# Kernel tuning notes

Hardware: AMD Instinct MI355X
Metric: run time of the kernel (lower is better)

The kernel has to match this reference:

```python
import jax, jax.numpy as jnp
import numpy as np
from jax.ops import segment_sum

N_NODES = 100000


def _add_self_loops(edge_index, n):
    loop = jnp.arange(n, dtype=edge_index.dtype)
    src = jnp.concatenate([edge_index[0], loop])
    dst = jnp.concatenate([edge_index[1], loop])
    return src, dst


def gcn_conv(x, W, b, src, dst, n):
    # PyG GCNConv: h = x @ W, symmetric-normalized sum aggregation, + bias
    h = x @ W                                        # [N, out]
    deg = segment_sum(jnp.ones_like(dst, dtype=h.dtype), dst, num_segments=n)
    dinv = jnp.where(deg > 0, jax.lax.rsqrt(deg), 0.0)  # deg^-1/2, inf->0
    w = dinv[src] * dinv[dst]                        # [E]
    msg = h[src] * w[:, None]                        # gather + scale
    agg = segment_sum(msg, dst, num_segments=n)      # scatter-add
    return agg + b


def setup_inputs() -> dict:
    key = jax.random.key(0)
    ks = jax.random.split(key, 10)
    in_c, hid = 128, 64
    x = jax.random.normal(ks[0], (N_NODES, in_c), dtype=jnp.float32)
    edge_index = jax.random.randint(ks[1], (2, 3200000), 0, N_NODES, dtype=jnp.int64)
    s = 0.1
    return {
        "x": x,
        "edge_index": edge_index,
        "W1": jax.random.normal(ks[2], (in_c, hid), dtype=jnp.float32) * s,
        "b1": jnp.zeros((hid,), dtype=jnp.float32),
        "W2": jax.random.normal(ks[3], (hid, hid // 2), dtype=jnp.float32) * s,
        "b2": jnp.zeros((hid // 2,), dtype=jnp.float32),
        "fc_w": jax.random.normal(ks[4], (hid // 2, hid // 2), dtype=jnp.float32) * s,
        "fc_b": jnp.zeros((hid // 2,), dtype=jnp.float32),
        "out_w": jax.random.normal(ks[5], (hid // 2, 2), dtype=jnp.float32) * s,
        "out_b": jnp.zeros((2,), dtype=jnp.float32),
    }


def reference(x, edge_index, W1, b1, W2, b2, fc_w, fc_b, out_w, out_b):
    n = x.shape[0]
    src, dst = _add_self_loops(edge_index, n)
    h = jax.nn.relu(gcn_conv(x, W1, b1, src, dst, n))   # dropout: eval mode, identity
    h = jax.nn.relu(gcn_conv(h, W2, b2, src, dst, n))
    h = jax.nn.relu(h @ fc_w + fc_b)
    return h @ out_w + out_b                             # [N, 2] logits
```

## Files before the change

### kernel.cpp

```cpp
#include <hip/hip_runtime.h>

#define WG 256
#define BN 128
#define NBMAX 800
#define CHUNK 8192

typedef unsigned int uint32;

__device__ inline ushort f2bf(float f) {
  uint32 u = __float_as_uint(f);
  return (ushort)((u + 0x7fffu + ((u >> 16) & 1u)) >> 16);
}
__device__ inline float bflo(uint32 v) { return __uint_as_float(v << 16); }
__device__ inline float bfhi(uint32 v) { return __uint_as_float(v & 0xffff0000u); }

__device__ inline bool detect_i64(const uint32* ei) {
  uint32 acc = 0;
#pragma unroll
  for (int i = 0; i < 8; i++) acc |= ei[2 * i + 1];
  return acc == 0u;
}

__global__ __launch_bounds__(WG) void k_bin(const int* __restrict__ ei,
                                            int* __restrict__ cursor,
                                            uint32* __restrict__ pairs,
                                            int NB, int E, int CAP) {
  __shared__ int hc[NBMAX];
  __shared__ int curs[NBMAX];
  const int c = blockIdx.x;
  for (int b = threadIdx.x; b < NB; b += WG) hc[b] = 0;
  __syncthreads();
  const bool i64 = detect_i64((const uint32*)ei);
  const int e0 = c * CHUNK;
  for (int i = 0; i < CHUNK; i += WG) {
    int e = e0 + i + threadIdx.x;
    if (e < E) {
      int d = i64 ? ei[2 * (E + e)] : ei[E + e];
      atomicAdd(&hc[d / BN], 1);
    }
  }
  __syncthreads();
  for (int b = threadIdx.x; b < NB; b += WG) {
    int cnt = hc[b];
    int base = 0;
    if (cnt > 0) base = atomicAdd(&cursor[b], cnt);
    curs[b] = b * CAP + base;
  }
  __syncthreads();
  for (int i = 0; i < CHUNK; i += WG) {
    int e = e0 + i + threadIdx.x;
    if (e < E) {
      int s, d;
      if (i64) { s = ei[2 * e]; d = ei[2 * (E + e)]; }
      else     { s = ei[e];     d = ei[E + e]; }
      int b = d / BN;
      int pos = atomicAdd(&curs[b], 1);
      if (pos < (b + 1) * CAP)
        pairs[pos] = ((uint32)s << 7) | (uint32)(d & (BN - 1));
    }
  }
}

__global__ __launch_bounds__(WG) void k_bsort(const uint32* __restrict__ pairs,
                                              const int* __restrict__ cursor,
                                              int* __restrict__ perm,
                                              int* __restrict__ rowbeg,
                                              int* __restrict__ rowend,
                                              float* __restrict__ dinv,
                                              int N, int CAP) {
  __shared__ int cnt[BN];
  __shared__ int cur[BN];
  __shared__ int sc[BN];
  const int b = blockIdx.x;
  const int t = threadIdx.x;
  if (t < BN) cnt[t] = 0;
  __syncthreads();
  const int beg = b * CAP;
  int cb = cursor[b];
  const int end = beg + (cb < CAP ? cb : CAP);
  for (int e = beg + t; e < end; e += WG)
    atomicAdd(&cnt[pairs[e] & (BN - 1)], 1);
  __syncthreads();
  if (t < BN) sc[t] = cnt[t];
  __syncthreads();
  for (int off = 1; off < BN; off <<= 1) {
    int v = (t < BN && t >= off) ? sc[t - off] : 0;
    __syncthreads();
    if (t < BN) sc[t] += v;
    __syncthreads();
  }
  if (t < BN) {
    int excl = beg + sc[t] - cnt[t];
    cur[t] = excl;
    int n = b * BN + t;
    if (n < N) {
      rowbeg[n] = excl;
      rowend[n] = excl + cnt[t];
      dinv[n] = rsqrtf((float)(cnt[t] + 1));
    }
  }
  __syncthreads();
  for (int e = beg + t; e < end; e += WG) {
    uint32 p = pairs[e];
    int pos = atomicAdd(&cur[p & (BN - 1)], 1);
    perm[pos] = (int)(p >> 7);
  }
}

__global__ __launch_bounds__(WG) void k_gemm1(const float* __restrict__ x,
                                              const float* __restrict__ W1,
                                              const float* __restrict__ dinv,
                                              uint32* __restrict__ ht1, int N) {
  __shared__ float xs[64 * 128];
  __shared__ float w1s[128 * 64];
  const int tid = threadIdx.x;
  const int n0 = blockIdx.x * 64;

  for (int v = tid; v < 2048; v += WG)
    *(float4*)&w1s[v * 4] = ((const float4*)W1)[v];
  for (int v = tid; v < 2048; v += WG) {
    int row = v >> 5, c4 = v & 31;
    int n = n0 + row;
    float4 val = make_float4(0.f, 0.f, 0.f, 0.f);
    if (n < N) val = ((const float4*)x)[(size_t)n * 32 + c4];
    *(float4*)&xs[row * 128 + ((c4 ^ ((row >> 2) & 3)) << 2)] = val;
  }
  __syncthreads();

  const int cg = tid & 15;
  const int ng = tid >> 4;
  const int ngm = ng & 3;
  float acc[4][4] = {};

#pragma unroll 4
  for (int k4 = 0; k4 < 32; k4++) {
    float4 xa[4], wv[4];
#pragma unroll
    for (int i = 0; i < 4; i++)
      xa[i] = *(const float4*)&xs[(ng * 4 + i) * 128 + ((k4 ^ ngm) << 2)];
#pragma unroll
    for (int kk = 0; kk < 4; kk++)
      wv[kk] = *(const float4*)&w1s[(k4 * 4 + kk) * 64 + cg * 4];
#pragma unroll
    for (int i = 0; i < 4; i++) {
#pragma unroll
      for (int kk = 0; kk < 4; kk++) {
        float a = (kk == 0) ? xa[i].x : (kk == 1) ? xa[i].y : (kk == 2) ? xa[i].z : xa[i].w;
        acc[i][0] += a * wv[kk].x;
        acc[i][1] += a * wv[kk].y;
        acc[i][2] += a * wv[kk].z;
        acc[i][3] += a * wv[kk].w;
      }
    }
  }

#pragma unroll
  for (int i = 0; i < 4; i++) {
    int n = n0 + ng * 4 + i;
    if (n >= N) continue;
    float dv = dinv[n];
    uint32 u01 = ((uint32)f2bf(acc[i][1] * dv) << 16) | f2bf(acc[i][0] * dv);
    uint32 u23 = ((uint32)f2bf(acc[i][3] * dv) << 16) | f2bf(acc[i][2] * dv);
    ((uint2*)ht1)[(size_t)n * 16 + cg] = make_uint2(u01, u23);
  }
}

__global__ __launch_bounds__(WG) void k_agg64b(const int* __restrict__ rowbeg,
                                               const int* __restrict__ rowend,
                                               const int* __restrict__ perm,
                                               const float* __restrict__ dinv,
                                               const uint32* __restrict__ ht,
                                               float* __restrict__ agg, int N) {
  int n = (blockIdx.x * WG + threadIdx.x) >> 6;
  int lane = threadIdx.x & 63;
  if (n >= N) return;
  const int sub = lane >> 5;
  const int cp = lane & 31;
  int beg = rowbeg[n], end = rowend[n];
  float a0 = 0.f, a1 = 0.f;
  if (sub == 0) {
    uint32 v = ht[(size_t)n * 32 + cp];
    a0 += bflo(v); a1 += bfhi(v);
  }
  int j = beg;
  for (; j + 16 <= end; j += 16) {
    int s[8];
    uint32 v[8];
#pragma unroll
    for (int u = 0; u < 8; u++) s[u] = perm[j + 2 * u + sub];
#pragma unroll
    for (int u = 0; u < 8; u++) v[u] = ht[(size_t)s[u] * 32 + cp];
#pragma unroll
    for (int u = 0; u < 8; u++) { a0 += bflo(v[u]); a1 += bfhi(v[u]); }
  }
  for (; j + 2 <= end; j += 2) {
    int s = perm[j + sub];
    uint32 v = ht[(size_t)s * 32 + cp];
    a0 += bflo(v); a1 += bfhi(v);
  }
  if (j < end && sub == 0) {
    int s = perm[j];
    uint32 v = ht[(size_t)s * 32 + cp];
    a0 += bflo(v); a1 += bfhi(v);
  }
  a0 += __shfl_xor(a0, 32, 64);
  a1 += __shfl_xor(a1, 32, 64);
  if (sub == 0) {
    float dv = dinv[n];
    ((float2*)agg)[(size_t)n * 32 + cp] = make_float2(a0 * dv, a1 * dv);
  }
}

__global__ __launch_bounds__(WG) void k_gemm2(const float* __restrict__ agg1,
                                              const float* __restrict__ b1,
                                              const float* __restrict__ W2,
                                              const float* __restrict__ dinv,
                                              uint32* __restrict__ ht2, int N) {
  __shared__ float as[64 * 68];
  __shared__ float w2s[64 * 32];
  const int tid = threadIdx.x;
  const int n0 = blockIdx.x * 64;

  for (int v = tid; v < 512; v += WG)
    *(float4*)&w2s[v * 4] = ((const float4*)W2)[v];
  for (int v = tid; v < 1024; v += WG) {
    int row = v >> 4, c4 = v & 15;
    int n = n0 + row;
    float4 val = make_float4(0.f, 0.f, 0.f, 0.f);
    if (n < N) {
      float4 g = ((const float4*)agg1)[(size_t)n * 16 + c4];
      float4 bb = ((const float4*)b1)[c4];
      val.x = fmaxf(g.x + bb.x, 0.f);
      val.y = fmaxf(g.y + bb.y, 0.f);
      val.z = fmaxf(g.z + bb.z, 0.f);
      val.w = fmaxf(g.w + bb.w, 0.f);
    }
    *(float4*)&as[row * 68 + c4 * 4] = val;
  }
  __syncthreads();

  const int cg = tid & 15;
  const int ng = tid >> 4;
  float acc[4][2] = {};

#pragma unroll 4
  for (int k4 = 0; k4 < 16; k4++) {
    float4 xa[4];
    float2 wv[4];
#pragma unroll
    for (int i = 0; i < 4; i++)
      xa[i] = *(const float4*)&as[(ng * 4 + i) * 68 + k4 * 4];
#pragma unroll
    for (int kk = 0; kk < 4; kk++)
      wv[kk] = *(const float2*)&w2s[(k4 * 4 + kk) * 32 + cg * 2];
#pragma unroll
    for (int i = 0; i < 4; i++) {
#pragma unroll
      for (int kk = 0; kk < 4; kk++) {
        float a = (kk == 0) ? xa[i].x : (kk == 1) ? xa[i].y : (kk == 2) ? xa[i].z : xa[i].w;
        acc[i][0] += a * wv[kk].x;
        acc[i][1] += a * wv[kk].y;
      }
    }
  }

#pragma unroll
  for (int i = 0; i < 4; i++) {
    int n = n0 + ng * 4 + i;
    if (n >= N) continue;
    float dv = dinv[n];
    ht2[(size_t)n * 16 + cg] =
        ((uint32)f2bf(acc[i][1] * dv) << 16) | f2bf(acc[i][0] * dv);
  }
}

__global__ __launch_bounds__(WG) void k_agg32h(const int* __restrict__ rowbeg,
                                               const int* __restrict__ rowend,
                                               const int* __restrict__ perm,
                                               const float* __restrict__ dinv,
                                               const uint32* __restrict__ ht,
                                               const float* __restrict__ b2,
                                               const float* __restrict__ fc_w,
                                               const float* __restrict__ fc_b,
                                               const float* __restrict__ out_w,
                                               const float* __restrict__ out_b,
                                               float* __restrict__ out, int N) {
  __shared__ float fcs[32 * 32];
  __shared__ float b2s[32], fcbs[32], ows[64];
  const int tid = threadIdx.x;
  ((float4*)fcs)[tid] = ((const float4*)fc_w)[tid];
  if (tid < 32) { b2s[tid] = b2[tid]; fcbs[tid] = fc_b[tid]; }
  if (tid < 64) ows[tid] = out_w[tid];
  __syncthreads();

  const int n = blockIdx.x * 4 + (tid >> 6);
  if (n >= N) return;
  const int lane = tid & 63;
  const int sub = lane >> 4;
  const int cp = lane & 15;
  int beg = rowbeg[n], end = rowend[n];
  float a0 = 0.f, a1 = 0.f;
  if (sub == 0) {
    uint32 v = ht[(size_t)n * 16 + cp];
    a0 += bflo(v); a1 += bfhi(v);
  }
  int j = beg;
  for (; j + 16 <= end; j += 16) {
    int s[4];
    uint32 v[4];
#pragma unroll
    for (int u = 0; u < 4; u++) s[u] = perm[j + 4 * u + sub];
#pragma unroll
    for (int u = 0; u < 4; u++) v[u] = ht[(size_t)s[u] * 16 + cp];
#pragma unroll
    for (int u = 0; u < 4; u++) { a0 += bflo(v[u]); a1 += bfhi(v[u]); }
  }
  for (; j + 4 <= end; j += 4) {
    int s = perm[j + sub];
    uint32 v = ht[(size_t)s * 16 + cp];
    a0 += bflo(v); a1 += bfhi(v);
  }
  if (j + sub < end) {
    int s = perm[j + sub];
    uint32 v = ht[(size_t)s * 16 + cp];
    a0 += bflo(v); a1 += bfhi(v);
  }
  a0 += __shfl_xor(a0, 16, 64);
  a1 += __shfl_xor(a1, 16, 64);
  a0 += __shfl_xor(a0, 32, 64);
  a1 += __shfl_xor(a1, 32, 64);
  float dv = dinv[n];
  float hp0 = fmaxf(a0 * dv + b2s[2 * cp], 0.f);
  float hp1 = fmaxf(a1 * dv + b2s[2 * cp + 1], 0.f);

  const int jj = lane & 31;
  float acc = fcbs[jj];
#pragma unroll
  for (int k = 0; k < 32; k++) {
    float hk = __shfl((k & 1) ? hp1 : hp0, k >> 1, 64);
    acc += hk * fcs[k * 32 + jj];
  }
  float t = fmaxf(acc, 0.f);
  float o0 = t * ows[2 * jj];
  float o1 = t * ows[2 * jj + 1];
#pragma unroll
  for (int off = 1; off <= 16; off <<= 1) {
    o0 += __shfl_xor(o0, off, 64);
    o1 += __shfl_xor(o1, off, 64);
  }
  if (lane == 0)
    ((float2*)out)[n] = make_float2(o0 + out_b[0], o1 + out_b[1]);
}

extern "C" void kernel_launch(void* const* d_in, const int* in_sizes, int n_in,
                              void* d_out, int out_size, void* d_ws, size_t ws_size,
                              hipStream_t stream) {
  const float* x   = (const float*)d_in[0];
  const int*   ei  = (const int*)d_in[1];
  const float* W1  = (const float*)d_in[2];
  const float* b1  = (const float*)d_in[3];
  const float* W2  = (const float*)d_in[4];
  const float* b2  = (const float*)d_in[5];
  const float* fcw = (const float*)d_in[6];
  const float* fcb = (const float*)d_in[7];
  const float* ow  = (const float*)d_in[8];
  const float* ob  = (const float*)d_in[9];

  const int N  = in_sizes[0] / 128;
  const int E  = in_sizes[1] / 2;
  const int NB = (N + BN - 1) / BN;
  const int NC = (E + CHUNK - 1) / CHUNK;
  const int CAP = (int)(((long long)E * BN) / N) + 1024;

  char* p = (char*)d_ws;
  int* cursor = (int*)p;             p += ((size_t)NB + 16) * 4;
  p = (char*)(((uintptr_t)p + 63) & ~(uintptr_t)63);
  uint32* pairs = (uint32*)p;        p += (size_t)NB * CAP * 4 + 64;
  int* perm = (int*)p;               p += (size_t)NB * CAP * 4 + 64;
  int* rowbeg = (int*)p;             p += (size_t)N * 4 + 64;
  int* rowend = (int*)p;             p += (size_t)N * 4 + 64;
  float* dinv = (float*)p;           p += (size_t)N * 4 + 64;
  p = (char*)(((uintptr_t)p + 63) & ~(uintptr_t)63);
  uint32* ht1 = (uint32*)p;          p += (size_t)N * 32 * 4;
  float* agg1 = (float*)p;           p += (size_t)N * 64 * 4;
  uint32* ht2 = (uint32*)p;          p += (size_t)N * 16 * 4;
  float* out = (float*)d_out;

  hipMemsetAsync(cursor, 0, (size_t)NB * sizeof(int), stream);
  hipLaunchKernelGGL(k_bin, dim3(NC), dim3(WG), 0, stream,
                     ei, cursor, pairs, NB, E, CAP);
  hipLaunchKernelGGL(k_bsort, dim3(NB), dim3(WG), 0, stream,
                     pairs, cursor, perm, rowbeg, rowend, dinv, N, CAP);
  hipLaunchKernelGGL(k_gemm1, dim3((N + 63) / 64), dim3(WG), 0, stream,
                     x, W1, dinv, ht1, N);
  {
    long long tot = (long long)N * 64;
    hipLaunchKernelGGL(k_agg64b, dim3((int)((tot + WG - 1) / WG)), dim3(WG), 0,
                       stream, rowbeg, rowend, perm, dinv, ht1, agg1, N);
  }
  hipLaunchKernelGGL(k_gemm2, dim3((N + 63) / 64), dim3(WG), 0, stream,
                     agg1, b1, W2, dinv, ht2, N);
  hipLaunchKernelGGL(k_agg32h, dim3((N + 3) / 4), dim3(WG), 0, stream,
                     rowbeg, rowend, perm, dinv, ht2,
                     b2, fcw, fcb, ow, ob, out, N);
}
```

Before: 318.6 us.

## Widen gather loads in aggregation and split final MLP into separate kernel

The layer-1 aggregation now has each lane load 8-byte uint2 chunks, so 16 lanes cover a row and four edges are processed per wave step. The layer-2 aggregation+MLP kernel is split into a pure gather kernel with 8 lanes per row and a separate per-node MLP kernel that stages rows in shared memory. The goal is more edges in flight per wave and less shuffle overhead in the dense epilogue. In exchange it adds an extra kernel launch, an fp32 agg2 round trip through memory that reuses the pairs buffer, and a smaller binning CHUNK.

```diff
diff --git a/kernel.cpp b/kernel.cpp
--- a/kernel.cpp
+++ b/kernel.cpp
@@ -3,7 +3,7 @@
 #define WG 256
 #define BN 128
 #define NBMAX 800
-#define CHUNK 8192
+#define CHUNK 4096
 
 typedef unsigned int uint32;
 
@@ -174,40 +174,102 @@
   int n = (blockIdx.x * WG + threadIdx.x) >> 6;
   int lane = threadIdx.x & 63;
   if (n >= N) return;
-  const int sub = lane >> 5;
-  const int cp = lane & 31;
+  const int sub = lane >> 4;
+  const int cp = lane & 15;
+  const uint2* __restrict__ tab = (const uint2*)ht;
   int beg = rowbeg[n], end = rowend[n];
-  float a0 = 0.f, a1 = 0.f;
+  float a0 = 0.f, a1 = 0.f, a2 = 0.f, a3 = 0.f;
   if (sub == 0) {
-    uint32 v = ht[(size_t)n * 32 + cp];
-    a0 += bflo(v); a1 += bfhi(v);
+    uint2 v = tab[(size_t)n * 16 + cp];
+    a0 += bflo(v.x); a1 += bfhi(v.x); a2 += bflo(v.y); a3 += bfhi(v.y);
   }
   int j = beg;
   for (; j + 16 <= end; j += 16) {
-    int s[8];
-    uint32 v[8];
-#pragma unroll
-    for (int u = 0; u < 8; u++) s[u] = perm[j + 2 * u + sub];
-#pragma unroll
-    for (int u = 0; u < 8; u++) v[u] = ht[(size_t)s[u] * 32 + cp];
-#pragma unroll
-    for (int u = 0; u < 8; u++) { a0 += bflo(v[u]); a1 += bfhi(v[u]); }
-  }
-  for (; j + 2 <= end; j += 2) {
+    int s[4];
+    uint2 v[4];
+#pragma unroll
+    for (int u = 0; u < 4; u++) s[u] = perm[j + 4 * u + sub];
+#pragma unroll
+    for (int u = 0; u < 4; u++) v[u] = tab[(size_t)s[u] * 16 + cp];
+#pragma unroll
+    for (int u = 0; u < 4; u++) {
+      a0 += bflo(v[u].x); a1 += bfhi(v[u].x);
+      a2 += bflo(v[u].y); a3 += bfhi(v[u].y);
+    }
+  }
+  for (; j + 4 <= end; j += 4) {
     int s = perm[j + sub];
-    uint32 v = ht[(size_t)s * 32 + cp];
-    a0 += bflo(v); a1 += bfhi(v);
-  }
-  if (j < end && sub == 0) {
-    int s = perm[j];
-    uint32 v = ht[(size_t)s * 32 + cp];
-    a0 += bflo(v); a1 += bfhi(v);
-  }
-  a0 += __shfl_xor(a0, 32, 64);
-  a1 += __shfl_xor(a1, 32, 64);
+    uint2 v = tab[(size_t)s * 16 + cp];
+    a0 += bflo(v.x); a1 += bfhi(v.x); a2 += bflo(v.y); a3 += bfhi(v.y);
+  }
+  if (j + sub < end) {
+    int s = perm[j + sub];
+    uint2 v = tab[(size_t)s * 16 + cp];
+    a0 += bflo(v.x); a1 += bfhi(v.x); a2 += bflo(v.y); a3 += bfhi(v.y);
+  }
+  a0 += __shfl_xor(a0, 16, 64); a1 += __shfl_xor(a1, 16, 64);
+  a2 += __shfl_xor(a2, 16, 64); a3 += __shfl_xor(a3, 16, 64);
+  a0 += __shfl_xor(a0, 32, 64); a1 += __shfl_xor(a1, 32, 64);
+  a2 += __shfl_xor(a2, 32, 64); a3 += __shfl_xor(a3, 32, 64);
   if (sub == 0) {
     float dv = dinv[n];
-    ((float2*)agg)[(size_t)n * 32 + cp] = make_float2(a0 * dv, a1 * dv);
+    ((float4*)agg)[(size_t)n * 16 + cp] =
+        make_float4(a0 * dv, a1 * dv, a2 * dv, a3 * dv);
+  }
+}
+
+__global__ __launch_bounds__(WG) void k_agg32b(const int* __restrict__ rowbeg,
+                                               const int* __restrict__ rowend,
+                                               const int* __restrict__ perm,
+                                               const float* __restrict__ dinv,
+                                               const uint32* __restrict__ ht,
+                                               float* __restrict__ agg, int N) {
+  int n = (blockIdx.x * WG + threadIdx.x) >> 6;
+  int lane = threadIdx.x & 63;
+  if (n >= N) return;
+  const int sub = lane >> 3;
+  const int cp = lane & 7;
+  const uint2* __restrict__ tab = (const uint2*)ht;
+  int beg = rowbeg[n], end = rowend[n];
+  float a0 = 0.f, a1 = 0.f, a2 = 0.f, a3 = 0.f;
+  if (sub == 0) {
+    uint2 v = tab[(size_t)n * 8 + cp];
+    a0 += bflo(v.x); a1 += bfhi(v.x); a2 += bflo(v.y); a3 += bfhi(v.y);
+  }
+  int j = beg;
+  for (; j + 16 <= end; j += 16) {
+    int s[2];
+    uint2 v[2];
+#pragma unroll
+    for (int u = 0; u < 2; u++) s[u] = perm[j + 8 * u + sub];
+#pragma unroll
+    for (int u = 0; u < 2; u++) v[u] = tab[(size_t)s[u] * 8 + cp];
+#pragma unroll
+    for (int u = 0; u < 2; u++) {
+      a0 += bflo(v[u].x); a1 += bfhi(v[u].x);
+      a2 += bflo(v[u].y); a3 += bfhi(v[u].y);
+    }
+  }
+  for (; j + 8 <= end; j += 8) {
+    int s = perm[j + sub];
+    uint2 v = tab[(size_t)s * 8 + cp];
+    a0 += bflo(v.x); a1 += bfhi(v.x); a2 += bflo(v.y); a3 += bfhi(v.y);
+  }
+  if (j + sub < end) {
+    int s = perm[j + sub];
+    uint2 v = tab[(size_t)s * 8 + cp];
+    a0 += bflo(v.x); a1 += bfhi(v.x); a2 += bflo(v.y); a3 += bfhi(v.y);
+  }
+  a0 += __shfl_xor(a0, 8, 64);  a1 += __shfl_xor(a1, 8, 64);
+  a2 += __shfl_xor(a2, 8, 64);  a3 += __shfl_xor(a3, 8, 64);
+  a0 += __shfl_xor(a0, 16, 64); a1 += __shfl_xor(a1, 16, 64);
+  a2 += __shfl_xor(a2, 16, 64); a3 += __shfl_xor(a3, 16, 64);
+  a0 += __shfl_xor(a0, 32, 64); a1 += __shfl_xor(a1, 32, 64);
+  a2 += __shfl_xor(a2, 32, 64); a3 += __shfl_xor(a3, 32, 64);
+  if (sub == 0) {
+    float dv = dinv[n];
+    ((float4*)agg)[(size_t)n * 8 + cp] =
+        make_float4(a0 * dv, a1 * dv, a2 * dv, a3 * dv);
   }
 }
 
@@ -274,82 +336,58 @@
   }
 }
 
-__global__ __launch_bounds__(WG) void k_agg32h(const int* __restrict__ rowbeg,
-                                               const int* __restrict__ rowend,
-                                               const int* __restrict__ perm,
-                                               const float* __restrict__ dinv,
-                                               const uint32* __restrict__ ht,
-                                               const float* __restrict__ b2,
-                                               const float* __restrict__ fc_w,
-                                               const float* __restrict__ fc_b,
-                                               const float* __restrict__ out_w,
-                                               const float* __restrict__ out_b,
-                                               float* __restrict__ out, int N) {
+__global__ __launch_bounds__(WG) void k_final(const float* __restrict__ agg2,
+                                              const float* __restrict__ b2,
+                                              const float* __restrict__ fc_w,
+                                              const float* __restrict__ fc_b,
+                                              const float* __restrict__ out_w,
+                                              const float* __restrict__ out_b,
+                                              float* __restrict__ out, int N) {
+  __shared__ float hs[256 * 33];
   __shared__ float fcs[32 * 32];
   __shared__ float b2s[32], fcbs[32], ows[64];
   const int tid = threadIdx.x;
+  const int n0 = blockIdx.x * 256;
+
   ((float4*)fcs)[tid] = ((const float4*)fc_w)[tid];
-  if (tid < 32) { b2s[tid] = b2[tid]; fcbs[tid] = fc_b[tid]; }
+  if (tid < 32) {
+    b2s[tid] = b2[tid];
+    fcbs[tid] = fc_b[tid];
+  }
   if (tid < 64) ows[tid] = out_w[tid];
-  __syncthreads();
-
-  const int n = blockIdx.x * 4 + (tid >> 6);
-  if (n >= N) return;
-  const int lane = tid & 63;
-  const int sub = lane >> 4;
-  const int cp = lane & 15;
-  int beg = rowbeg[n], end = rowend[n];
-  float a0 = 0.f, a1 = 0.f;
-  if (sub == 0) {
-    uint32 v = ht[(size_t)n * 16 + cp];
-    a0 += bflo(v); a1 += bfhi(v);
-  }
-  int j = beg;
-  for (; j + 16 <= end; j += 16) {
-    int s[4];
-    uint32 v[4];
-#pragma unroll
-    for (int u = 0; u < 4; u++) s[u] = perm[j + 4 * u + sub];
-#pragma unroll
-    for (int u = 0; u < 4; u++) v[u] = ht[(size_t)s[u] * 16 + cp];
-#pragma unroll
-    for (int u = 0; u < 4; u++) { a0 += bflo(v[u]); a1 += bfhi(v[u]); }
-  }
-  for (; j + 4 <= end; j += 4) {
-    int s = perm[j + sub];
-    uint32 v = ht[(size_t)s * 16 + cp];
-    a0 += bflo(v); a1 += bfhi(v);
-  }
-  if (j + sub < end) {
-    int s = perm[j + sub];
-    uint32 v = ht[(size_t)s * 16 + cp];
-    a0 += bflo(v); a1 += bfhi(v);
-  }
-  a0 += __shfl_xor(a0, 16, 64);
-  a1 += __shfl_xor(a1, 16, 64);
-  a0 += __shfl_xor(a0, 32, 64);
-  a1 += __shfl_xor(a1, 32, 64);
-  float dv = dinv[n];
-  float hp0 = fmaxf(a0 * dv + b2s[2 * cp], 0.f);
-  float hp1 = fmaxf(a1 * dv + b2s[2 * cp + 1], 0.f);
-
-  const int jj = lane & 31;
-  float acc = fcbs[jj];
+  for (int v = tid; v < 2048; v += WG) {
+    int row = v >> 3, c4 = v & 7;
+    int n = n0 + row;
+    float4 val = make_float4(0.f, 0.f, 0.f, 0.f);
+    if (n < N) val = ((const float4*)agg2)[(size_t)n * 8 + c4];
+    float* p = &hs[row * 33 + c4 * 4];
+    p[0] = val.x; p[1] = val.y; p[2] = val.z; p[3] = val.w;
+  }
+  __syncthreads();
+
+  int n = n0 + tid;
+  float acc[32] = {};
+  const int base = tid * 33;
 #pragma unroll
   for (int k = 0; k < 32; k++) {
-    float hk = __shfl((k & 1) ? hp1 : hp0, k >> 1, 64);
-    acc += hk * fcs[k * 32 + jj];
-  }
-  float t = fmaxf(acc, 0.f);
-  float o0 = t * ows[2 * jj];
-  float o1 = t * ows[2 * jj + 1];
-#pragma unroll
-  for (int off = 1; off <= 16; off <<= 1) {
-    o0 += __shfl_xor(o0, off, 64);
-    o1 += __shfl_xor(o1, off, 64);
-  }
-  if (lane == 0)
-    ((float2*)out)[n] = make_float2(o0 + out_b[0], o1 + out_b[1]);
+    float vk = fmaxf(hs[base + k] + b2s[k], 0.f);
+#pragma unroll
+    for (int j4 = 0; j4 < 8; j4++) {
+      float4 f = *(const float4*)&fcs[k * 32 + j4 * 4];
+      acc[j4 * 4 + 0] += vk * f.x;
+      acc[j4 * 4 + 1] += vk * f.y;
+      acc[j4 * 4 + 2] += vk * f.z;
+      acc[j4 * 4 + 3] += vk * f.w;
+    }
+  }
+  float o0 = out_b[0], o1 = out_b[1];
+#pragma unroll
+  for (int j = 0; j < 32; j++) {
+    float t = fmaxf(acc[j] + fcbs[j], 0.f);
+    o0 += t * ows[2 * j];
+    o1 += t * ows[2 * j + 1];
+  }
+  if (n < N) ((float2*)out)[n] = make_float2(o0, o1);
 }
 
 extern "C" void kernel_launch(void* const* d_in, const int* in_sizes, int n_in,
@@ -375,7 +413,8 @@
   char* p = (char*)d_ws;
   int* cursor = (int*)p;             p += ((size_t)NB + 16) * 4;
   p = (char*)(((uintptr_t)p + 63) & ~(uintptr_t)63);
-  uint32* pairs = (uint32*)p;        p += (size_t)NB * CAP * 4 + 64;
+  uint32* pairs = (uint32*)p;
+  float* agg2 = (float*)p;           p += (size_t)NB * CAP * 4 + 64;
   int* perm = (int*)p;               p += (size_t)NB * CAP * 4 + 64;
   int* rowbeg = (int*)p;             p += (size_t)N * 4 + 64;
   int* rowend = (int*)p;             p += (size_t)N * 4 + 64;
@@ -400,7 +439,11 @@
   }
   hipLaunchKernelGGL(k_gemm2, dim3((N + 63) / 64), dim3(WG), 0, stream,
                      agg1, b1, W2, dinv, ht2, N);
-  hipLaunchKernelGGL(k_agg32h, dim3((N + 3) / 4), dim3(WG), 0, stream,
-                     rowbeg, rowend, perm, dinv, ht2,
-                     b2, fcw, fcb, ow, ob, out, N);
-}
+  {
+    long long tot = (long long)N * 64;
+    hipLaunchKernelGGL(k_agg32b, dim3((int)((tot + WG - 1) / WG)), dim3(WG), 0,
+                       stream, rowbeg, rowend, perm, dinv, ht2, agg2, N);
+  }
+  hipLaunchKernelGGL(k_final, dim3((N + 255) / 256), dim3(WG), 0, stream,
+                     agg2, b2, fcw, fcb, ow, ob, out, N);
+}
```

After: 293.3 us. -7.9%, faster.
